# Optimization experiments

Measured on AMD Instinct MI355X. Metric: run time of the kernel, lower is better.

Reference implementation:

```python
import jax, jax.numpy as jnp
import numpy as np

H, D = 16, 64  # num_heads, head_dim (hidden=1024)


def _rel_shift(x):
    # Transformer-XL skewing: x [B,H,T,L] -> shifted [B,H,T,T]
    B, Hh, T, L = x.shape
    x = jnp.pad(x, ((0, 0), (0, 0), (0, 0), (1, 0)))
    x = x.reshape(B, Hh, L + 1, T)[:, :, 1:, :]
    return x.reshape(B, Hh, T, L)[:, :, :, :T]


def setup_inputs() -> dict:
    key = jax.random.key(0)
    ks = jax.random.split(key, 9)
    B, T, hid = 2, 2048, 1024
    s = 0.02
    return {
        "x": jax.random.normal(ks[0], (B, T, hid), jnp.float32),
        "pos_emb": jax.random.normal(ks[1], (T, hid), jnp.float32),
        "Wq": jax.random.normal(ks[2], (hid, hid), jnp.float32) * s,
        "Wk": jax.random.normal(ks[3], (hid, hid), jnp.float32) * s,
        "Wv": jax.random.normal(ks[4], (hid, hid), jnp.float32) * s,
        "Wo": jax.random.normal(ks[5], (hid, hid), jnp.float32) * s,
        "Wrel": jax.random.normal(ks[6], (hid, hid), jnp.float32) * s,
        "bias_u": jax.random.normal(ks[7], (H, D), jnp.float32) * s,
        "bias_v": jax.random.normal(ks[8], (H, D), jnp.float32) * s,
    }


def reference(x, pos_emb, Wq, Wk, Wv, Wo, Wrel, bias_u, bias_v):
    B, T, hid = x.shape
    scale = D ** (-0.5)
    # projections (torch Linear: y = x @ W.T), reshape to [B,H,T,D]
    q = (x @ Wq.T).reshape(B, T, H, D).transpose(0, 2, 1, 3)
    k = (x @ Wk.T).reshape(B, T, H, D).transpose(0, 2, 1, 3)
    v = (x @ Wv.T).reshape(B, T, H, D).transpose(0, 2, 1, 3)
    # content score with bias_u
    content = jnp.einsum('bhtd,bhsd->bhts', q + bias_u[None, :, None, :], k)
    # positional score with bias_v against projected relative keys [H,L,D]
    rel_k = (pos_emb @ Wrel.T).reshape(-1, H, D).transpose(1, 0, 2)
    pos_score = jnp.einsum('bhtd,hld->bhtl', q + bias_v[None, :, None, :], rel_k)
    pos_score = _rel_shift(pos_score)
    scores = (content + pos_score) * scale
    attn = jax.nn.softmax(scores, axis=-1)
    out = jnp.einsum('bhts,bhsd->bhtd', attn, v)
    out = out.transpose(0, 2, 1, 3).reshape(B, T, hid)
    return out @ Wo.T
```

## Files before the change

kernel.cpp:

```cpp
#include <hip/hip_runtime.h>
#include <hip/hip_bf16.h>

#define T_SEQ 2048
#define HID   1024
#define NH    16
#define HD    64
#define NB    2

typedef __bf16 bf16_t;
typedef bf16_t bf16x8 __attribute__((ext_vector_type(8)));
typedef bf16_t bf16x4 __attribute__((ext_vector_type(4)));
typedef float  f32x4  __attribute__((ext_vector_type(4)));

static __device__ __forceinline__ f32x4 mfma16(bf16x8 a, bf16x8 b, f32x4 c) {
    return __builtin_amdgcn_mfma_f32_16x16x32_bf16(a, b, c, 0, 0, 0);
}

static __device__ __forceinline__ void gll16(const bf16_t* g, bf16_t* l) {
    __builtin_amdgcn_global_load_lds(
        (const __attribute__((address_space(1))) void*)g,
        (__attribute__((address_space(3))) void*)l, 16, 0, 0);
}

__global__ __launch_bounds__(256) void cvt_all(
    const float* __restrict__ x, const float* __restrict__ pos,
    const float* __restrict__ wq, const float* __restrict__ wk,
    const float* __restrict__ wv, const float* __restrict__ wo,
    const float* __restrict__ wrel,
    bf16_t* __restrict__ xb, bf16_t* __restrict__ pb,
    bf16_t* __restrict__ wqb, bf16_t* __restrict__ wkb,
    bf16_t* __restrict__ wvb, bf16_t* __restrict__ wob,
    bf16_t* __restrict__ wrelb)
{
    int blk = blockIdx.x;
    const float* in; bf16_t* out;
    if (blk < 2048)      { in = x;   out = xb; }
    else if (blk < 3072) { in = pos; out = pb; blk -= 2048; }
    else {
        const int wi = (blk - 3072) >> 9; blk = (blk - 3072) & 511;
        switch (wi) {
            case 0:  in = wq;   out = wqb;   break;
            case 1:  in = wk;   out = wkb;   break;
            case 2:  in = wv;   out = wvb;   break;
            case 3:  in = wo;   out = wob;   break;
            default: in = wrel; out = wrelb; break;
        }
    }
    const int i = blk * 256 + threadIdx.x;
    const float4* p = (const float4*)(in + (size_t)i * 8);
    float4 a0 = p[0], a1 = p[1];
    bf16x8 v;
    v[0]=(bf16_t)a0.x; v[1]=(bf16_t)a0.y; v[2]=(bf16_t)a0.z; v[3]=(bf16_t)a0.w;
    v[4]=(bf16_t)a1.x; v[5]=(bf16_t)a1.y; v[6]=(bf16_t)a1.z; v[7]=(bf16_t)a1.w;
    *(bf16x8*)(out + (size_t)i * 8) = v;
}

static __device__ __forceinline__ void gemm_core(
    bf16_t* Al, bf16_t* Bl,
    const bf16_t* __restrict__ A, const bf16_t* __restrict__ W,
    void* __restrict__ outv, int row0, int col0, int omode)
{
    const int tid = threadIdx.x;
    const int w = tid >> 6, lane = tid & 63;
    const int wr = (w >> 1) * 64, wc = (w & 1) * 64;
    const int lr = lane & 15, lkg = lane >> 4;
    const int kd = lkg * 8;
    const int rsh   = lane >> 3;
    const int colSw = ((lane & 7) * 8) ^ (rsh << 3);
    const int rBase = 8*w + rsh;

    f32x4 acc[4][4] = {};

#pragma unroll
    for (int i = 0; i < 4; ++i) {
        const int r = rBase + 32*i;
        gll16(A + (size_t)(row0 + r)*HID + colSw, &Al[i*2048 + w*512]);
        gll16(W + (size_t)(col0 + r)*HID + colSw, &Bl[i*2048 + w*512]);
    }
    __syncthreads();

    for (int t = 0; t < 16; ++t) {
        const int cur = (t & 1) * 8192;
        const int nxt = 8192 - cur;
        if (t < 15) {
            const int k0 = (t + 1) * 64;
#pragma unroll
            for (int i = 0; i < 4; ++i) {
                const int r = rBase + 32*i;
                gll16(A + (size_t)(row0 + r)*HID + k0 + colSw, &Al[nxt + i*2048 + w*512]);
                gll16(W + (size_t)(col0 + r)*HID + k0 + colSw, &Bl[nxt + i*2048 + w*512]);
            }
        }
#pragma unroll
        for (int ks = 0; ks < 2; ++ks) {
            bf16x8 af[4], bq[4];
#pragma unroll
            for (int i = 0; i < 4; ++i) {
                const int ar = wr + i*16 + lr;
                af[i] = *(const bf16x8*)&Al[cur + ar*64 + ((ks*32 + kd) ^ ((ar & 7) << 3))];
                const int br = wc + i*16 + lr;
                bq[i] = *(const bf16x8*)&Bl[cur + br*64 + ((ks*32 + kd) ^ ((br & 7) << 3))];
            }
#pragma unroll
            for (int i = 0; i < 4; ++i)
#pragma unroll
                for (int j = 0; j < 4; ++j)
                    acc[i][j] = mfma16(af[i], bq[j], acc[i][j]);
        }
        __syncthreads();
    }

    const int rb = lkg * 4;
#pragma unroll
    for (int i = 0; i < 4; ++i) {
#pragma unroll
        for (int j = 0; j < 4; ++j) {
            const int col = col0 + wc + j*16 + lr;
            const int row = row0 + wr + i*16 + rb;
            if (omode == 0) {
                bf16_t* ob = (bf16_t*)outv;
#pragma unroll
                for (int r = 0; r < 4; ++r)
                    ob[(size_t)(row + r) * HID + col] = (bf16_t)acc[i][j][r];
            } else if (omode == 1) {
                const int bb = row >> 11, tt = row & (T_SEQ - 1);
                const int hh = col >> 6,  d = col & 63;
                bf16x4 pk;
#pragma unroll
                for (int r = 0; r < 4; ++r) pk[r] = (bf16_t)acc[i][j][r];
                *(bf16x4*)((bf16_t*)outv + ((size_t)((bb*NH + hh)*HD + d))*T_SEQ + tt) = pk;
            } else {
                float* of = (float*)outv;
#pragma unroll
                for (int r = 0; r < 4; ++r)
                    of[(size_t)(row + r) * HID + col] = acc[i][j][r];
            }
        }
    }
}

__global__ __launch_bounds__(256) void gemm_proj(
    const bf16_t* __restrict__ xb, const bf16_t* __restrict__ pb,
    const bf16_t* __restrict__ wqb, const bf16_t* __restrict__ wkb,
    const bf16_t* __restrict__ wvb, const bf16_t* __restrict__ wrelb,
    bf16_t* __restrict__ qb, bf16_t* __restrict__ kb,
    bf16_t* __restrict__ vtb, bf16_t* __restrict__ rkb)
{
    __shared__ bf16_t Al[2*128*64];
    __shared__ bf16_t Bl[2*128*64];
    const int hw = blockIdx.x;
    const int logical = (hw & 7) * 112 + (hw >> 3);
    const bf16_t* A; const bf16_t* W; void* out; int omode = 0; int l;
    if (logical < 256)      { A = xb; W = wqb;   out = qb;  l = logical; }
    else if (logical < 512) { A = xb; W = wkb;   out = kb;  l = logical - 256; }
    else if (logical < 768) { A = xb; W = wvb;   out = vtb; l = logical - 512; omode = 1; }
    else                    { A = pb; W = wrelb; out = rkb; l = logical - 768; }
    const int row0 = (l >> 3) * 128, col0 = (l & 7) * 128;
    gemm_core(Al, Bl, A, W, out, row0, col0, omode);
}

__global__ __launch_bounds__(256) void gemm_out(
    const bf16_t* __restrict__ ab, const bf16_t* __restrict__ wob,
    float* __restrict__ outp)
{
    __shared__ bf16_t Al[2*128*64];
    __shared__ bf16_t Bl[2*128*64];
    const int hw = blockIdx.x;
    const int logical = (hw & 7) * 32 + (hw >> 3);
    const int row0 = (logical >> 3) * 128, col0 = (logical & 7) * 128;
    gemm_core(Al, Bl, ab, wob, outp, row0, col0, 2);
}

__global__ __launch_bounds__(256) void attn_kernel(
    const bf16_t* __restrict__ Q, const bf16_t* __restrict__ K,
    const bf16_t* __restrict__ VT, const bf16_t* __restrict__ RK,
    const float* __restrict__ bias_u, const float* __restrict__ bias_v,
    bf16_t* __restrict__ AO)
{
    const int hw = blockIdx.x;
    const int logical = (hw & 7) * 128 + (hw >> 3);
    const int tile = logical & 31;
    const int h    = (logical >> 5) & 15;
    const int b    = logical >> 9;

    const int w = threadIdx.x >> 6, lane = threadIdx.x & 63;
    const int t0 = tile * 64;
    const int lr = lane & 15, lkg = lane >> 4;
    const int kd = lkg * 8;

    __shared__ bf16_t Kl[64*64];
    __shared__ bf16_t Vl[64*64];
    __shared__ bf16_t Rl[128*64];
    __shared__ bf16_t pp[4][16][84];
    __shared__ bf16_t pl[4][16][72];

    const int tb = t0 + w * 16;

    bf16x8 aqu[2], aqv[2], aqv2[2];
    {
        const int t  = tb + lr;
        const int t2 = (t + 1 < T_SEQ) ? t + 1 : T_SEQ - 1;
        const bf16_t* qp  = Q + ((size_t)(b*T_SEQ + t )*NH + h)*HD;
        const bf16_t* qp2 = Q + ((size_t)(b*T_SEQ + t2)*NH + h)*HD;
        const float* bu = bias_u + h*HD;
        const float* bv = bias_v + h*HD;
#pragma unroll
        for (int f = 0; f < 2; ++f) {
            const int k0 = f*32 + kd;
            bf16x8 q1 = *(const bf16x8*)(qp  + k0);
            bf16x8 q2 = *(const bf16x8*)(qp2 + k0);
#pragma unroll
            for (int j = 0; j < 8; ++j) {
                const float fu = bu[k0+j], fv = bv[k0+j];
                aqu [f][j] = (bf16_t)(((float)q1[j] + fu) * 0.125f);
                aqv [f][j] = (bf16_t)(((float)q1[j] + fv) * 0.125f);
                aqv2[f][j] = (bf16_t)(((float)q2[j] + fv) * 0.125f);
            }
        }
    }

    float m_run = -1e30f, l_run = 0.0f;
    f32x4 oacc[4];
    f32x4 zf = {0.f, 0.f, 0.f, 0.f};
#pragma unroll
    for (int nf = 0; nf < 4; ++nf) oacc[nf] = zf;

    const bf16_t* Kb = K  + (size_t)(b*T_SEQ)*HID + h*HD;
    const bf16_t* Vb = VT + (size_t)((b*NH + h)*HD)*T_SEQ;
    const bf16_t* Rb = RK + h*HD;
    const int d15 = 15 - lr;

    const int rsh   = lane >> 3;
    const int colSw = ((lane & 7) * 8) ^ (rsh << 3);
    const int kvRow = 16*w + rsh;
    const int rRow  = 32*w + rsh;

    for (int s0 = 0; s0 < T_SEQ; s0 += 64) {
        const int r1base = s0 - t0 + T_SEQ - 64;
        const int r2base = s0 - t0 - 65;
        const bool anyB1 = (s0 <= t0 + 63);
        const bool anyB2 = (s0 >= t0 - 61);

        __syncthreads();
#pragma unroll
        for (int i = 0; i < 2; ++i) {
            const int r = kvRow + 8*i;
            gll16(Kb + (size_t)(s0 + r)*HID + colSw, &Kl[(2*w + i)*512]);
            gll16(Vb + (size_t)r*T_SEQ + s0 + colSw, &Vl[(2*w + i)*512]);
        }
        {
            const int rb0 = anyB1 ? r1base : r2base;
#pragma unroll
            for (int i = 0; i < 4; ++i) {
                const long g = (long)(rb0 + rRow + 8*i);
                gll16(Rb + g*HID + colSw, &Rl[(4*w + i)*512]);
            }
        }
        __syncthreads();

        f32x4 sc[4];
#pragma unroll
        for (int j = 0; j < 4; ++j) {
            const int row = j*16 + lr;
            const int sw = (row & 7) << 3;
            bf16x8 a0 = *(const bf16x8*)&Kl[row*64 + (kd ^ sw)];
            bf16x8 a1 = *(const bf16x8*)&Kl[row*64 + ((32 + kd) ^ sw)];
            sc[j] = mfma16(a1, aqu[1], mfma16(a0, aqu[0], zf));
        }

        if (s0 <= tb + 15) {
#pragma unroll
            for (int jf = 0; jf < 5; ++jf) {
                const int rr = 48 - 16*w + jf*16 + lr;
                const int sw = (rr & 7) << 3;
                bf16x8 a0 = *(const bf16x8*)&Rl[rr*64 + (kd ^ sw)];
                bf16x8 a1 = *(const bf16x8*)&Rl[rr*64 + ((32 + kd) ^ sw)];
                f32x4 c = mfma16(a1, aqv[1], mfma16(a0, aqv[0], zf));
                bf16x4 cb;
#pragma unroll
                for (int r = 0; r < 4; ++r) cb[r] = (bf16_t)c[r];
                *(bf16x4*)&pp[w][lr][jf*16 + 4*lkg] = cb;
            }
            if (s0 <= tb - 63) {
#pragma unroll
                for (int j = 0; j < 4; ++j)
#pragma unroll
                    for (int r = 0; r < 4; ++r)
                        sc[j][r] += (float)pp[w][lr][16*j + 4*lkg + r + d15];
            } else {
#pragma unroll
                for (int j = 0; j < 4; ++j)
#pragma unroll
                    for (int r = 0; r < 4; ++r) {
                        const int sof = 16*j + 4*lkg + r;
                        const int dt  = (s0 + sof) - (tb + lr);
                        const float v = (float)pp[w][lr][sof + d15];
                        sc[j][r] += (dt <= 0) ? v : 0.0f;
                    }
            }
        }

        if (anyB1 && anyB2) {
            __syncthreads();
#pragma unroll
            for (int i = 0; i < 4; ++i) {
                const long g = (long)(r2base + rRow + 8*i);
                gll16(Rb + g*HID + colSw, &Rl[(4*w + i)*512]);
            }
            __syncthreads();
        }

        if (s0 >= tb - 61) {
#pragma unroll
            for (int jf = 0; jf < 5; ++jf) {
                const int rr = 48 - 16*w + jf*16 + lr;
                const int sw = (rr & 7) << 3;
                bf16x8 a0 = *(const bf16x8*)&Rl[rr*64 + (kd ^ sw)];
                bf16x8 a1 = *(const bf16x8*)&Rl[rr*64 + ((32 + kd) ^ sw)];
                f32x4 c = mfma16(a1, aqv2[1], mfma16(a0, aqv2[0], zf));
                bf16x4 cb;
#pragma unroll
                for (int r = 0; r < 4; ++r) cb[r] = (bf16_t)c[r];
                *(bf16x4*)&pp[w][lr][jf*16 + 4*lkg] = cb;
            }
            if (s0 >= tb + 17) {
#pragma unroll
                for (int j = 0; j < 4; ++j)
#pragma unroll
                    for (int r = 0; r < 4; ++r)
                        sc[j][r] += (float)pp[w][lr][16*j + 4*lkg + r + d15];
            } else {
#pragma unroll
                for (int j = 0; j < 4; ++j)
#pragma unroll
                    for (int r = 0; r < 4; ++r) {
                        const int sof = 16*j + 4*lkg + r;
                        const int dt  = (s0 + sof) - (tb + lr);
                        const float v = (float)pp[w][lr][sof + d15];
                        sc[j][r] += (dt >= 2) ? v : 0.0f;
                    }
            }
        }

        float mx = fmaxf(fmaxf(fmaxf(sc[0][0], sc[0][1]), fmaxf(sc[0][2], sc[0][3])),
                         fmaxf(fmaxf(sc[1][0], sc[1][1]), fmaxf(sc[1][2], sc[1][3])));
        mx = fmaxf(mx, fmaxf(fmaxf(fmaxf(sc[2][0], sc[2][1]), fmaxf(sc[2][2], sc[2][3])),
                             fmaxf(fmaxf(sc[3][0], sc[3][1]), fmaxf(sc[3][2], sc[3][3]))));
        mx = fmaxf(mx, __shfl_xor(mx, 16, 64));
        mx = fmaxf(mx, __shfl_xor(mx, 32, 64));
        const float mnew = fmaxf(m_run, mx);
        const float fac = __expf(m_run - mnew);
        float sum = 0.0f;
#pragma unroll
        for (int j = 0; j < 4; ++j) {
            bf16x4 pk;
#pragma unroll
            for (int r = 0; r < 4; ++r) {
                const float p = __expf(sc[j][r] - mnew);
                sum += p;
                pk[r] = (bf16_t)p;
            }
            *(bf16x4*)&pl[w][lr][16*j + 4*lkg] = pk;
        }
        sum += __shfl_xor(sum, 16, 64);
        sum += __shfl_xor(sum, 32, 64);
        l_run = l_run * fac + sum;
        m_run = mnew;

#pragma unroll
        for (int r = 0; r < 4; ++r) {
            const float facq = __shfl(fac, 4*lkg + r, 64);
#pragma unroll
            for (int nf = 0; nf < 4; ++nf) oacc[nf][r] *= facq;
        }

        bf16x8 pa0 = *(const bf16x8*)(&pl[w][lr][kd]);
        bf16x8 pa1 = *(const bf16x8*)(&pl[w][lr][32 + kd]);
#pragma unroll
        for (int nf = 0; nf < 4; ++nf) {
            const int row = nf*16 + lr;
            const int sw = (row & 7) << 3;
            bf16x8 b0 = *(const bf16x8*)&Vl[row*64 + (kd ^ sw)];
            bf16x8 b1 = *(const bf16x8*)&Vl[row*64 + ((32 + kd) ^ sw)];
            oacc[nf] = mfma16(pa1, b1, mfma16(pa0, b0, oacc[nf]));
        }
    }

    const float linv = 1.0f / l_run;
#pragma unroll
    for (int r = 0; r < 4; ++r) {
        const float lq = __shfl(linv, 4*lkg + r, 64);
        const int t = tb + 4*lkg + r;
#pragma unroll
        for (int nf = 0; nf < 4; ++nf)
            AO[(size_t)(b*T_SEQ + t)*HID + h*HD + nf*16 + lr] = (bf16_t)(oacc[nf][r] * lq);
    }
}

extern "C" void kernel_launch(void* const* d_in, const int* in_sizes, int n_in,
                              void* d_out, int out_size, void* d_ws, size_t ws_size,
                              hipStream_t stream) {
    const float* x    = (const float*)d_in[0];
    const float* pos  = (const float*)d_in[1];
    const float* Wq   = (const float*)d_in[2];
    const float* Wk   = (const float*)d_in[3];
    const float* Wv   = (const float*)d_in[4];
    const float* Wo   = (const float*)d_in[5];
    const float* Wrel = (const float*)d_in[6];
    const float* bu   = (const float*)d_in[7];
    const float* bv   = (const float*)d_in[8];

    bf16_t* ws   = (bf16_t*)d_ws;
    const size_t M1 = 1024u * 1024u;
    bf16_t* qb    = ws;
    bf16_t* kb    = ws + 4*M1;
    bf16_t* vtb   = ws + 8*M1;
    bf16_t* rkb   = ws + 12*M1;
    bf16_t* ab    = ws + 14*M1;
    bf16_t* xb    = ab;
    bf16_t* pb    = ws + 18*M1;
    bf16_t* wqb   = ws + 20*M1;
    bf16_t* wkb   = ws + 21*M1;
    bf16_t* wvb   = ws + 22*M1;
    bf16_t* wob   = ws + 23*M1;
    bf16_t* wrelb = ws + 24*M1;

    cvt_all<<<5632, 256, 0, stream>>>(x, pos, Wq, Wk, Wv, Wo, Wrel,
                                      xb, pb, wqb, wkb, wvb, wob, wrelb);

    gemm_proj<<<896, 256, 0, stream>>>(xb, pb, wqb, wkb, wvb, wrelb,
                                       qb, kb, vtb, rkb);

    attn_kernel<<<1024, 256, 0, stream>>>(qb, kb, vtb, rkb, bu, bv, ab);

    gemm_out<<<256, 256, 0, stream>>>(ab, wob, (float*)d_out);
}
```

Before: 273.6 us.

## Double R buffers to drop mid-loop syncs, keep positional scores fp32, skip rescale

The single shared R tile, which had to be reloaded for the second band with two extra barriers, becomes two separate R1/R2 shared buffers loaded together up front. Each tile iteration now has only the two loop barriers. Positional scores are kept in fp32 in the scratch buffer rather than rounded to bf16, and the online-softmax rescale of the accumulator is skipped when no lane's max grew. Global and LDS addresses are precomputed as incrementing pointers. The cost is roughly 16KB more LDS (doubled R buffer, fp32 pp), which may reduce occupancy.

```diff
diff --git a/kernel.cpp b/kernel.cpp
--- a/kernel.cpp
+++ b/kernel.cpp
@@ -190,8 +190,9 @@
 
     __shared__ bf16_t Kl[64*64];
     __shared__ bf16_t Vl[64*64];
-    __shared__ bf16_t Rl[128*64];
-    __shared__ bf16_t pp[4][16][84];
+    __shared__ bf16_t R1l[128*64];
+    __shared__ bf16_t R2l[128*64];
+    __shared__ float  pp[4][16][84];
     __shared__ bf16_t pl[4][16][72];
 
     const int tb = t0 + w * 16;
@@ -225,119 +226,108 @@
 #pragma unroll
     for (int nf = 0; nf < 4; ++nf) oacc[nf] = zf;
 
-    const bf16_t* Kb = K  + (size_t)(b*T_SEQ)*HID + h*HD;
-    const bf16_t* Vb = VT + (size_t)((b*NH + h)*HD)*T_SEQ;
-    const bf16_t* Rb = RK + h*HD;
-    const int d15 = 15 - lr;
+    const int lsw = (lr & 7) << 3;
+    const bf16_t* KlA = &Kl[lr*64 + (kd ^ lsw)];
+    const bf16_t* KlB = &Kl[lr*64 + ((32 + kd) ^ lsw)];
+    const bf16_t* VlA = &Vl[lr*64 + (kd ^ lsw)];
+    const bf16_t* VlB = &Vl[lr*64 + ((32 + kd) ^ lsw)];
+    const int rrow0 = 48 - 16*w + lr;
+    const bf16_t* R1A = &R1l[rrow0*64 + (kd ^ lsw)];
+    const bf16_t* R1B = &R1l[rrow0*64 + ((32 + kd) ^ lsw)];
+    const bf16_t* R2A = &R2l[rrow0*64 + (kd ^ lsw)];
+    const bf16_t* R2B = &R2l[rrow0*64 + ((32 + kd) ^ lsw)];
+    const float*  ppb = &pp[w][lr][4*lkg + 15 - lr];
+    float*        ppw = &pp[w][lr][4*lkg];
+    bf16_t*       plw = &pl[w][lr][4*lkg];
+    const bf16_t* plr = &pl[w][lr][0];
 
     const int rsh   = lane >> 3;
     const int colSw = ((lane & 7) * 8) ^ (rsh << 3);
     const int kvRow = 16*w + rsh;
     const int rRow  = 32*w + rsh;
+    const bf16_t* Kg  = K  + (size_t)(b*T_SEQ)*HID + h*HD + (size_t)kvRow*HID + colSw;
+    const bf16_t* Vg  = VT + (size_t)((b*NH + h)*HD)*T_SEQ + (size_t)kvRow*T_SEQ + colSw;
+    const bf16_t* Rb  = RK + h*HD;
+    const bf16_t* R1g = Rb + (ptrdiff_t)(T_SEQ - 64 - t0 + rRow)*HID + colSw;
+    const bf16_t* R2g = Rb + (ptrdiff_t)(-65 - t0 + rRow)*HID + colSw;
 
     for (int s0 = 0; s0 < T_SEQ; s0 += 64) {
-        const int r1base = s0 - t0 + T_SEQ - 64;
-        const int r2base = s0 - t0 - 65;
         const bool anyB1 = (s0 <= t0 + 63);
         const bool anyB2 = (s0 >= t0 - 61);
 
         __syncthreads();
 #pragma unroll
         for (int i = 0; i < 2; ++i) {
-            const int r = kvRow + 8*i;
-            gll16(Kb + (size_t)(s0 + r)*HID + colSw, &Kl[(2*w + i)*512]);
-            gll16(Vb + (size_t)r*T_SEQ + s0 + colSw, &Vl[(2*w + i)*512]);
-        }
-        {
-            const int rb0 = anyB1 ? r1base : r2base;
-#pragma unroll
-            for (int i = 0; i < 4; ++i) {
-                const long g = (long)(rb0 + rRow + 8*i);
-                gll16(Rb + g*HID + colSw, &Rl[(4*w + i)*512]);
-            }
+            gll16(Kg + (size_t)(8*i)*HID,   &Kl[(2*w + i)*512]);
+            gll16(Vg + (size_t)(8*i)*T_SEQ, &Vl[(2*w + i)*512]);
+        }
+        if (anyB1) {
+#pragma unroll
+            for (int i = 0; i < 4; ++i)
+                gll16(R1g + (size_t)(8*i)*HID, &R1l[(4*w + i)*512]);
+        }
+        if (anyB2) {
+#pragma unroll
+            for (int i = 0; i < 4; ++i)
+                gll16(R2g + (size_t)(8*i)*HID, &R2l[(4*w + i)*512]);
         }
         __syncthreads();
+        Kg  += (size_t)64*HID;
+        Vg  += 64;
+        R1g += (size_t)64*HID;
+        R2g += (size_t)64*HID;
 
         f32x4 sc[4];
 #pragma unroll
-        for (int j = 0; j < 4; ++j) {
-            const int row = j*16 + lr;
-            const int sw = (row & 7) << 3;
-            bf16x8 a0 = *(const bf16x8*)&Kl[row*64 + (kd ^ sw)];
-            bf16x8 a1 = *(const bf16x8*)&Kl[row*64 + ((32 + kd) ^ sw)];
-            sc[j] = mfma16(a1, aqu[1], mfma16(a0, aqu[0], zf));
-        }
+        for (int j = 0; j < 4; ++j)
+            sc[j] = mfma16(*(const bf16x8*)(KlB + j*1024), aqu[1],
+                     mfma16(*(const bf16x8*)(KlA + j*1024), aqu[0], zf));
+
+        const int dbase = s0 - tb + 4*lkg - lr;
 
         if (s0 <= tb + 15) {
 #pragma unroll
             for (int jf = 0; jf < 5; ++jf) {
-                const int rr = 48 - 16*w + jf*16 + lr;
-                const int sw = (rr & 7) << 3;
-                bf16x8 a0 = *(const bf16x8*)&Rl[rr*64 + (kd ^ sw)];
-                bf16x8 a1 = *(const bf16x8*)&Rl[rr*64 + ((32 + kd) ^ sw)];
-                f32x4 c = mfma16(a1, aqv[1], mfma16(a0, aqv[0], zf));
-                bf16x4 cb;
-#pragma unroll
-                for (int r = 0; r < 4; ++r) cb[r] = (bf16_t)c[r];
-                *(bf16x4*)&pp[w][lr][jf*16 + 4*lkg] = cb;
+                f32x4 c = mfma16(*(const bf16x8*)(R1B + jf*1024), aqv[1],
+                           mfma16(*(const bf16x8*)(R1A + jf*1024), aqv[0], zf));
+                *(f32x4*)(ppw + 16*jf) = c;
             }
             if (s0 <= tb - 63) {
 #pragma unroll
                 for (int j = 0; j < 4; ++j)
 #pragma unroll
                     for (int r = 0; r < 4; ++r)
-                        sc[j][r] += (float)pp[w][lr][16*j + 4*lkg + r + d15];
+                        sc[j][r] += ppb[16*j + r];
             } else {
 #pragma unroll
                 for (int j = 0; j < 4; ++j)
 #pragma unroll
                     for (int r = 0; r < 4; ++r) {
-                        const int sof = 16*j + 4*lkg + r;
-                        const int dt  = (s0 + sof) - (tb + lr);
-                        const float v = (float)pp[w][lr][sof + d15];
-                        sc[j][r] += (dt <= 0) ? v : 0.0f;
+                        const float v = ppb[16*j + r];
+                        sc[j][r] += (dbase + 16*j + r <= 0) ? v : 0.0f;
                     }
             }
         }
-
-        if (anyB1 && anyB2) {
-            __syncthreads();
-#pragma unroll
-            for (int i = 0; i < 4; ++i) {
-                const long g = (long)(r2base + rRow + 8*i);
-                gll16(Rb + g*HID + colSw, &Rl[(4*w + i)*512]);
-            }
-            __syncthreads();
-        }
-
         if (s0 >= tb - 61) {
 #pragma unroll
             for (int jf = 0; jf < 5; ++jf) {
-                const int rr = 48 - 16*w + jf*16 + lr;
-                const int sw = (rr & 7) << 3;
-                bf16x8 a0 = *(const bf16x8*)&Rl[rr*64 + (kd ^ sw)];
-                bf16x8 a1 = *(const bf16x8*)&Rl[rr*64 + ((32 + kd) ^ sw)];
-                f32x4 c = mfma16(a1, aqv2[1], mfma16(a0, aqv2[0], zf));
-                bf16x4 cb;
-#pragma unroll
-                for (int r = 0; r < 4; ++r) cb[r] = (bf16_t)c[r];
-                *(bf16x4*)&pp[w][lr][jf*16 + 4*lkg] = cb;
+                f32x4 c = mfma16(*(const bf16x8*)(R2B + jf*1024), aqv2[1],
+                           mfma16(*(const bf16x8*)(R2A + jf*1024), aqv2[0], zf));
+                *(f32x4*)(ppw + 16*jf) = c;
             }
             if (s0 >= tb + 17) {
 #pragma unroll
                 for (int j = 0; j < 4; ++j)
 #pragma unroll
                     for (int r = 0; r < 4; ++r)
-                        sc[j][r] += (float)pp[w][lr][16*j + 4*lkg + r + d15];
+                        sc[j][r] += ppb[16*j + r];
             } else {
 #pragma unroll
                 for (int j = 0; j < 4; ++j)
 #pragma unroll
                     for (int r = 0; r < 4; ++r) {
-                        const int sof = 16*j + 4*lkg + r;
-                        const int dt  = (s0 + sof) - (tb + lr);
-                        const float v = (float)pp[w][lr][sof + d15];
-                        sc[j][r] += (dt >= 2) ? v : 0.0f;
+                        const float v = ppb[16*j + r];
+                        sc[j][r] += (dbase + 16*j + r >= 2) ? v : 0.0f;
                     }
             }
         }
@@ -349,7 +339,10 @@
         mx = fmaxf(mx, __shfl_xor(mx, 16, 64));
         mx = fmaxf(mx, __shfl_xor(mx, 32, 64));
         const float mnew = fmaxf(m_run, mx);
-        const float fac = __expf(m_run - mnew);
+        const bool resc = !__all(mx <= m_run);
+        float fac = 1.0f;
+        if (resc) fac = __expf(m_run - mnew);
+        m_run = mnew;
         float sum = 0.0f;
 #pragma unroll
         for (int j = 0; j < 4; ++j) {
@@ -360,30 +353,26 @@
                 sum += p;
                 pk[r] = (bf16_t)p;
             }
-            *(bf16x4*)&pl[w][lr][16*j + 4*lkg] = pk;
+            *(bf16x4*)(plw + 16*j) = pk;
         }
         sum += __shfl_xor(sum, 16, 64);
         sum += __shfl_xor(sum, 32, 64);
         l_run = l_run * fac + sum;
-        m_run = mnew;
-
-#pragma unroll
-        for (int r = 0; r < 4; ++r) {
-            const float facq = __shfl(fac, 4*lkg + r, 64);
-#pragma unroll
-            for (int nf = 0; nf < 4; ++nf) oacc[nf][r] *= facq;
-        }
-
-        bf16x8 pa0 = *(const bf16x8*)(&pl[w][lr][kd]);
-        bf16x8 pa1 = *(const bf16x8*)(&pl[w][lr][32 + kd]);
-#pragma unroll
-        for (int nf = 0; nf < 4; ++nf) {
-            const int row = nf*16 + lr;
-            const int sw = (row & 7) << 3;
-            bf16x8 b0 = *(const bf16x8*)&Vl[row*64 + (kd ^ sw)];
-            bf16x8 b1 = *(const bf16x8*)&Vl[row*64 + ((32 + kd) ^ sw)];
-            oacc[nf] = mfma16(pa1, b1, mfma16(pa0, b0, oacc[nf]));
-        }
+        if (resc) {
+#pragma unroll
+            for (int r = 0; r < 4; ++r) {
+                const float facq = __shfl(fac, 4*lkg + r, 64);
+#pragma unroll
+                for (int nf = 0; nf < 4; ++nf) oacc[nf][r] *= facq;
+            }
+        }
+
+        bf16x8 pa0 = *(const bf16x8*)(plr + kd);
+        bf16x8 pa1 = *(const bf16x8*)(plr + 32 + kd);
+#pragma unroll
+        for (int nf = 0; nf < 4; ++nf)
+            oacc[nf] = mfma16(pa1, *(const bf16x8*)(VlB + nf*1024),
+                        mfma16(pa0, *(const bf16x8*)(VlA + nf*1024), oacc[nf]));
     }
 
     const float linv = 1.0f / l_run;
```

Measured after the change: 227.0 us, median of 2. 1.21x faster.
